# Kernel tuning notes

Measured on AMD Instinct MI355X. Metric: run time of the kernel, lower is better.

The kernel has to match this reference:

```python
import jax, jax.numpy as jnp
import numpy as np

B = 1048576


def _normalize_rotation_matrix(R):
    # Faithful to torch: U, S, V = svd(R); Rn = U @ V^T; flip whole U by sign(det); recompute.
    U, S, Vh = jnp.linalg.svd(R)  # R = U diag(S) Vh, so torch's V^T == Vh
    Rn = jnp.matmul(U, Vh)
    det = jnp.linalg.det(Rn)[:, None, None]
    sign = jnp.sign(det)
    U = U * sign
    return jnp.matmul(U, Vh)


def _quat_to_rotmat(q):
    # q: [B, 4] as (w, x, y, z); same element layout as the torch loop, vectorized.
    w, x, y, z = q[:, 0], q[:, 1], q[:, 2], q[:, 3]
    R = jnp.stack([
        1 - 2 * (y ** 2 + z ** 2), 2 * (x * y - w * z),     2 * (x * z + w * y),
        2 * (x * y + w * z),       1 - 2 * (x ** 2 + z ** 2), 2 * (y * z - w * x),
        2 * (x * z - w * y),       2 * (y * z + w * x),     1 - 2 * (x ** 2 + y ** 2),
    ], axis=-1)
    return R.reshape(-1, 3, 3)


def setup_inputs() -> dict:
    key = jax.random.key(0)
    k1, k2, k3 = jax.random.split(key, 3)
    pred_R = jax.random.normal(k1, (B, 3, 3), dtype=jnp.float32)
    pred_t = jax.random.normal(k2, (B, 1, 3), dtype=jnp.float32)
    gt_transform = jax.random.normal(k3, (B, 7), dtype=jnp.float32)
    return {"pred_R": pred_R, "pred_t": pred_t, "gt_transform": gt_transform}


def reference(pred_R, pred_t, gt_transform):
    gt_quat = gt_transform[:, :4]
    igt_t = gt_transform[:, 4:]
    igt_R = _quat_to_rotmat(gt_quat)              # [B,3,3]
    igt_R = _normalize_rotation_matrix(igt_R)
    pred_Rn = _normalize_rotation_matrix(pred_R)
    # matmul(pred_R^T, igt_R): [b,i,k] = sum_j pred_Rn[b,j,i] * igt_R[b,j,k]
    M = jnp.einsum('bji,bjk->bik', pred_Rn, igt_R)
    eye = jnp.eye(3, dtype=M.dtype)
    rot_loss = jnp.mean((M - eye) ** 2)
    t_loss = jnp.mean((pred_t - igt_t[:, None, :]) ** 2)
    return rot_loss + t_loss
```

## Files before the change

### kernel.cpp

```cpp
#include <hip/hip_runtime.h>


#define TILE 256
#define TPB_TILES 4
#define SCALED_ITERS 3
#define PLAIN_ITERS  1

__device__ __forceinline__ float se3_elem(const float* __restrict__ R,
                                          const float* __restrict__ Q,
                                          const float* __restrict__ T)
{
    float w  = Q[0], x = Q[1], y = Q[2], z = Q[3];

    float v2 = x*x + y*y + z*z;
    float c  = 1.0f - 2.0f*v2;
    float r2 = fmaxf(c*c + 4.0f*(w*w)*v2, 1e-30f);
    float rr = __builtin_amdgcn_rsqf(r2);
    float ga = c * rr;
    float gt_ = (1.0f - ga) * __builtin_amdgcn_rcpf(fmaxf(v2, 1e-37f));
    float gb = 2.0f * w * rr;

    float tx = gt_*x, ty = gt_*y, tz = gt_*z;
    float bx = gb*x,  by = gb*y,  bz = gb*z;

    float G0 = ga + tx*x,  G1 = tx*y - bz,   G2 = tx*z + by;
    float G3 = tx*y + bz,  G4 = ga + ty*y,   G5 = ty*z - bx;
    float G6 = tx*z - by,  G7 = ty*z + bx,   G8 = ga + tz*z;

    float X0 = R[0], X1 = R[1], X2 = R[2];
    float X3 = R[3], X4 = R[4], X5 = R[5];
    float X6 = R[6], X7 = R[7], X8 = R[8];

    float s = 1.0f;
#pragma unroll
    for (int it = 0; it < SCALED_ITERS + PLAIN_ITERS; ++it) {
        float C0 = X4*X8 - X5*X7;
        float C1 = X5*X6 - X3*X8;
        float C2 = X3*X7 - X4*X6;
        float C3 = X2*X7 - X1*X8;
        float C4 = X0*X8 - X2*X6;
        float C5 = X1*X6 - X0*X7;
        float C6 = X1*X5 - X2*X4;
        float C7 = X2*X3 - X0*X5;
        float C8 = X0*X4 - X1*X3;
        float det = X0*C0 + X1*C1 + X2*C2;
        if (it == 0) s = (det < 0.0f) ? -1.0f : 1.0f;
        float ka, kb;
        if (it < SCALED_ITERS) {
            float ad = fminf(fmaxf(fabsf(det), 1e-30f), 1e30f);
            float g  = __builtin_amdgcn_exp2f(0.33333333f * __builtin_amdgcn_logf(ad));
            ka = 0.5f * __builtin_amdgcn_rcpf(g);
            kb = 0.5f * g * __builtin_amdgcn_rcpf(det);
        } else {
            ka = 0.5f;
            kb = 0.5f * __builtin_amdgcn_rcpf(det);
        }
        if (it == SCALED_ITERS + PLAIN_ITERS - 1) { ka *= s; kb *= s; }
        X0 = ka*X0 + kb*C0;  X1 = ka*X1 + kb*C1;  X2 = ka*X2 + kb*C2;
        X3 = ka*X3 + kb*C3;  X4 = ka*X4 + kb*C4;  X5 = ka*X5 + kb*C5;
        X6 = ka*X6 + kb*C6;  X7 = ka*X7 + kb*C7;  X8 = ka*X8 + kb*C8;
    }

    float d0 = G0-X0, d1 = G1-X1, d2 = G2-X2;
    float d3 = G3-X3, d4 = G4-X4, d5 = G5-X5;
    float d6 = G6-X6, d7 = G7-X7, d8 = G8-X8;
    float rot = d0*d0 + d1*d1 + d2*d2
              + d3*d3 + d4*d4 + d5*d5
              + d6*d6 + d7*d7 + d8*d8;

    float e0 = T[0] - Q[4];
    float e1 = T[1] - Q[5];
    float e2 = T[2] - Q[6];
    float tl = e0*e0 + e1*e1 + e2*e2;

    return rot * (1.0f/9.0f) + tl * (1.0f/3.0f);
}

__global__ __launch_bounds__(256) void se3_partial_kernel(
    const float* __restrict__ pred_R,
    const float* __restrict__ pred_t,
    const float* __restrict__ gt,
    float* __restrict__ partials, int B, float invB)
{
    __shared__ __align__(16) float ldsR[2][TILE * 9];
    __shared__ __align__(16) float ldsQ[2][TILE * 7];
    __shared__ __align__(16) float ldsT[2][TILE * 3];
    __shared__ float wsums[4];

    const int tid     = threadIdx.x;
    const int ntiles  = (B + TILE - 1) / TILE;
    const int tile0   = blockIdx.x * TPB_TILES;

    float acc = 0.0f;

    float4 r0, r1, r2, q0, q1, t0;

    auto load_tile = [&](int tile) {
        const float4* sR = reinterpret_cast<const float4*>(pred_R) + (size_t)tile * (TILE * 9 / 4);
        const float4* sQ = reinterpret_cast<const float4*>(gt)     + (size_t)tile * (TILE * 7 / 4);
        const float4* sT = reinterpret_cast<const float4*>(pred_t) + (size_t)tile * (TILE * 3 / 4);
        r0 = sR[tid];
        r1 = sR[tid + 256];
        if (tid < 64)  r2 = sR[tid + 512];
        q0 = sQ[tid];
        if (tid < 192) { q1 = sQ[tid + 256]; t0 = sT[tid]; }
    };
    auto store_tile = [&](int buf) {
        float4* dR = reinterpret_cast<float4*>(ldsR[buf]);
        float4* dQ = reinterpret_cast<float4*>(ldsQ[buf]);
        float4* dT = reinterpret_cast<float4*>(ldsT[buf]);
        dR[tid]       = r0;
        dR[tid + 256] = r1;
        if (tid < 64)  dR[tid + 512] = r2;
        dQ[tid]       = q0;
        if (tid < 192) { dQ[tid + 256] = q1; dT[tid] = t0; }
    };

    const bool all_full = (tile0 + TPB_TILES) * TILE <= B;

    if (all_full) {
        load_tile(tile0);
        store_tile(0);
        __syncthreads();
#pragma unroll
        for (int lt = 0; lt < TPB_TILES; ++lt) {
            if (lt + 1 < TPB_TILES) load_tile(tile0 + lt + 1);
            const int buf = lt & 1;
            acc += se3_elem(&ldsR[buf][9 * tid],
                            &ldsQ[buf][7 * tid],
                            &ldsT[buf][3 * tid]);
            __syncthreads();
            if (lt + 1 < TPB_TILES) {
                store_tile((lt + 1) & 1);
                __syncthreads();
            }
        }
        acc *= invB;
    } else {
        for (int lt = 0; lt < TPB_TILES; ++lt) {
            const int tile = tile0 + lt;
            if (tile >= ntiles) break;
            const int base  = tile * TILE;
            int count = B - base;
            if (count > TILE) count = TILE;
            __syncthreads();
            for (int i = tid; i < count * 9; i += 256) ldsR[0][i] = pred_R[(size_t)base * 9 + i];
            for (int i = tid; i < count * 7; i += 256) ldsQ[0][i] = gt[(size_t)base * 7 + i];
            for (int i = tid; i < count * 3; i += 256) ldsT[0][i] = pred_t[(size_t)base * 3 + i];
            __syncthreads();
            if (tid < count)
                acc += se3_elem(&ldsR[0][9 * tid], &ldsQ[0][7 * tid], &ldsT[0][3 * tid]);
        }
        acc *= invB;
    }

#pragma unroll
    for (int off = 32; off > 0; off >>= 1)
        acc += __shfl_down(acc, off, 64);

    int lane = tid & 63;
    int wid  = tid >> 6;
    if (lane == 0) wsums[wid] = acc;
    __syncthreads();
    if (tid == 0)
        partials[blockIdx.x] = wsums[0] + wsums[1] + wsums[2] + wsums[3];
}

__global__ __launch_bounds__(256) void se3_reduce_kernel(
    const float* __restrict__ partials, float* __restrict__ out, int n)
{
    float acc = 0.0f;
    for (int i = threadIdx.x; i < n; i += 256)
        acc += partials[i];

#pragma unroll
    for (int off = 32; off > 0; off >>= 1)
        acc += __shfl_down(acc, off, 64);

    __shared__ float wsums[4];
    int lane = threadIdx.x & 63;
    int wid  = threadIdx.x >> 6;
    if (lane == 0) wsums[wid] = acc;
    __syncthreads();
    if (threadIdx.x == 0)
        out[0] = wsums[0] + wsums[1] + wsums[2] + wsums[3];
}

__global__ __launch_bounds__(256) void se3_atomic_kernel(
    const float* __restrict__ pred_R,
    const float* __restrict__ pred_t,
    const float* __restrict__ gt,
    float* __restrict__ out, int B, float invB)
{
    __shared__ __align__(16) float ldsR[TILE * 9];
    __shared__ __align__(16) float ldsQ[TILE * 7];
    __shared__ __align__(16) float ldsT[TILE * 3];
    __shared__ float wsums[4];

    const int tid  = threadIdx.x;
    const int base = blockIdx.x * TILE;
    int count = B - base;
    if (count > TILE) count = TILE;

    for (int i = tid; i < count * 9; i += 256) ldsR[i] = pred_R[(size_t)base * 9 + i];
    for (int i = tid; i < count * 7; i += 256) ldsQ[i] = gt[(size_t)base * 7 + i];
    for (int i = tid; i < count * 3; i += 256) ldsT[i] = pred_t[(size_t)base * 3 + i];
    __syncthreads();

    float acc = 0.0f;
    if (tid < count)
        acc = se3_elem(&ldsR[9 * tid], &ldsQ[7 * tid], &ldsT[3 * tid]) * invB;

#pragma unroll
    for (int off = 32; off > 0; off >>= 1)
        acc += __shfl_down(acc, off, 64);

    int lane = tid & 63;
    int wid  = tid >> 6;
    if (lane == 0) wsums[wid] = acc;
    __syncthreads();
    if (tid == 0)
        atomicAdd(out, wsums[0] + wsums[1] + wsums[2] + wsums[3]);
}

extern "C" void kernel_launch(void* const* d_in, const int* in_sizes, int n_in,
                              void* d_out, int out_size, void* d_ws, size_t ws_size,
                              hipStream_t stream) {
    const float* pred_R = (const float*)d_in[0];
    const float* pred_t = (const float*)d_in[1];
    const float* gt     = (const float*)d_in[2];
    float* out = (float*)d_out;
    int B = in_sizes[0] / 9;

    const int block  = 256;
    const int ntiles = (B + TILE - 1) / TILE;
    const int grid   = (ntiles + TPB_TILES - 1) / TPB_TILES;

    if (d_ws != nullptr && ws_size >= (size_t)grid * sizeof(float)) {
        float* partials = (float*)d_ws;
        se3_partial_kernel<<<grid, block, 0, stream>>>(pred_R, pred_t, gt,
                                                       partials, B,
                                                       1.0f / (float)B);
        se3_reduce_kernel<<<1, block, 0, stream>>>(partials, out, grid);
    } else {
        hipMemsetAsync(out, 0, sizeof(float), stream);
        se3_atomic_kernel<<<ntiles, block, 0, stream>>>(pred_R, pred_t, gt,
                                                        out, B, 1.0f / (float)B);
    }
}
```

Measured before the change: 106.5 us.

## Replace two-kernel partial reduction with atomics and double tiles per block

Drops the separate partials write and single-block reduce kernel in favor of a memset plus direct atomicAdd from each block, emitting two atomics per block (mid-loop and end). Tiles per block double from 4 to 8, halving grid size. This removes a second kernel launch and its serial single-block tail, at the cost of a memset launch, atomic contention on one address, and nondeterministic float summation order.

```diff
diff --git a/kernel.cpp b/kernel.cpp
--- a/kernel.cpp
+++ b/kernel.cpp
@@ -2,7 +2,7 @@
 
 
 #define TILE 256
-#define TPB_TILES 4
+#define TPB_TILES 8
 #define SCALED_ITERS 3
 #define PLAIN_ITERS  1
 
@@ -76,20 +76,21 @@
     return rot * (1.0f/9.0f) + tl * (1.0f/3.0f);
 }
 
-__global__ __launch_bounds__(256) void se3_partial_kernel(
+__global__ __launch_bounds__(256) void se3_loss_kernel(
     const float* __restrict__ pred_R,
     const float* __restrict__ pred_t,
     const float* __restrict__ gt,
-    float* __restrict__ partials, int B, float invB)
+    float* __restrict__ out, int B, float invB)
 {
     __shared__ __align__(16) float ldsR[2][TILE * 9];
     __shared__ __align__(16) float ldsQ[2][TILE * 7];
     __shared__ __align__(16) float ldsT[2][TILE * 3];
     __shared__ float wsums[4];
 
-    const int tid     = threadIdx.x;
-    const int ntiles  = (B + TILE - 1) / TILE;
-    const int tile0   = blockIdx.x * TPB_TILES;
+    const int tid    = threadIdx.x;
+    const int ntiles = (B + TILE - 1) / TILE;
+    const int tile0  = blockIdx.x * TPB_TILES;
+    if (tile0 >= ntiles) return;
 
     float acc = 0.0f;
 
@@ -115,6 +116,19 @@
         dQ[tid]       = q0;
         if (tid < 192) { dQ[tid + 256] = q1; dT[tid] = t0; }
     };
+    auto block_reduce_to0 = [&](float v) -> float {
+#pragma unroll
+        for (int off = 32; off > 0; off >>= 1)
+            v += __shfl_down(v, off, 64);
+        int lane = tid & 63;
+        int wid  = tid >> 6;
+        if (lane == 0) wsums[wid] = v;
+        __syncthreads();
+        float r = 0.0f;
+        if (tid == 0) r = wsums[0] + wsums[1] + wsums[2] + wsums[3];
+        __syncthreads();
+        return r;
+    };
 
     const bool all_full = (tile0 + TPB_TILES) * TILE <= B;
 
@@ -129,13 +143,19 @@
             acc += se3_elem(&ldsR[buf][9 * tid],
                             &ldsQ[buf][7 * tid],
                             &ldsT[buf][3 * tid]);
+            if (lt == TPB_TILES / 2 - 1) {
+                float p = block_reduce_to0(acc * invB);
+                if (tid == 0) atomicAdd(out, p);
+                acc = 0.0f;
+            }
             __syncthreads();
             if (lt + 1 < TPB_TILES) {
                 store_tile((lt + 1) & 1);
                 __syncthreads();
             }
         }
-        acc *= invB;
+        float p = block_reduce_to0(acc * invB);
+        if (tid == 0) atomicAdd(out, p);
     } else {
         for (int lt = 0; lt < TPB_TILES; ++lt) {
             const int tile = tile0 + lt;
@@ -151,76 +171,9 @@
             if (tid < count)
                 acc += se3_elem(&ldsR[0][9 * tid], &ldsQ[0][7 * tid], &ldsT[0][3 * tid]);
         }
-        acc *= invB;
+        float p = block_reduce_to0(acc * invB);
+        if (tid == 0) atomicAdd(out, p);
     }
-
-#pragma unroll
-    for (int off = 32; off > 0; off >>= 1)
-        acc += __shfl_down(acc, off, 64);
-
-    int lane = tid & 63;
-    int wid  = tid >> 6;
-    if (lane == 0) wsums[wid] = acc;
-    __syncthreads();
-    if (tid == 0)
-        partials[blockIdx.x] = wsums[0] + wsums[1] + wsums[2] + wsums[3];
-}
-
-__global__ __launch_bounds__(256) void se3_reduce_kernel(
-    const float* __restrict__ partials, float* __restrict__ out, int n)
-{
-    float acc = 0.0f;
-    for (int i = threadIdx.x; i < n; i += 256)
-        acc += partials[i];
-
-#pragma unroll
-    for (int off = 32; off > 0; off >>= 1)
-        acc += __shfl_down(acc, off, 64);
-
-    __shared__ float wsums[4];
-    int lane = threadIdx.x & 63;
-    int wid  = threadIdx.x >> 6;
-    if (lane == 0) wsums[wid] = acc;
-    __syncthreads();
-    if (threadIdx.x == 0)
-        out[0] = wsums[0] + wsums[1] + wsums[2] + wsums[3];
-}
-
-__global__ __launch_bounds__(256) void se3_atomic_kernel(
-    const float* __restrict__ pred_R,
-    const float* __restrict__ pred_t,
-    const float* __restrict__ gt,
-    float* __restrict__ out, int B, float invB)
-{
-    __shared__ __align__(16) float ldsR[TILE * 9];
-    __shared__ __align__(16) float ldsQ[TILE * 7];
-    __shared__ __align__(16) float ldsT[TILE * 3];
-    __shared__ float wsums[4];
-
-    const int tid  = threadIdx.x;
-    const int base = blockIdx.x * TILE;
-    int count = B - base;
-    if (count > TILE) count = TILE;
-
-    for (int i = tid; i < count * 9; i += 256) ldsR[i] = pred_R[(size_t)base * 9 + i];
-    for (int i = tid; i < count * 7; i += 256) ldsQ[i] = gt[(size_t)base * 7 + i];
-    for (int i = tid; i < count * 3; i += 256) ldsT[i] = pred_t[(size_t)base * 3 + i];
-    __syncthreads();
-
-    float acc = 0.0f;
-    if (tid < count)
-        acc = se3_elem(&ldsR[9 * tid], &ldsQ[7 * tid], &ldsT[3 * tid]) * invB;
-
-#pragma unroll
-    for (int off = 32; off > 0; off >>= 1)
-        acc += __shfl_down(acc, off, 64);
-
-    int lane = tid & 63;
-    int wid  = tid >> 6;
-    if (lane == 0) wsums[wid] = acc;
-    __syncthreads();
-    if (tid == 0)
-        atomicAdd(out, wsums[0] + wsums[1] + wsums[2] + wsums[3]);
 }
 
 extern "C" void kernel_launch(void* const* d_in, const int* in_sizes, int n_in,
@@ -232,19 +185,12 @@
     float* out = (float*)d_out;
     int B = in_sizes[0] / 9;
 
+    hipMemsetAsync(out, 0, sizeof(float), stream);
+
     const int block  = 256;
     const int ntiles = (B + TILE - 1) / TILE;
     const int grid   = (ntiles + TPB_TILES - 1) / TPB_TILES;
 
-    if (d_ws != nullptr && ws_size >= (size_t)grid * sizeof(float)) {
-        float* partials = (float*)d_ws;
-        se3_partial_kernel<<<grid, block, 0, stream>>>(pred_R, pred_t, gt,
-                                                       partials, B,
-                                                       1.0f / (float)B);
-        se3_reduce_kernel<<<1, block, 0, stream>>>(partials, out, grid);
-    } else {
-        hipMemsetAsync(out, 0, sizeof(float), stream);
-        se3_atomic_kernel<<<ntiles, block, 0, stream>>>(pred_R, pred_t, gt,
-                                                        out, B, 1.0f / (float)B);
-    }
+    se3_loss_kernel<<<grid, block, 0, stream>>>(pred_R, pred_t, gt, out, B,
+                                                1.0f / (float)B);
 }
```

New measurement: 108.4 us. Within noise of the previous version (+1.8%).
